# Kernel optimization log

Measured on AMD Instinct MI355X. Metric: run time of the kernel, lower is better.

## Reference

```python
import jax, jax.numpy as jnp
import numpy as np

B, L = 4, 2048
D_MODEL, D_STATE, D_CONV, EXPAND = 1024, 16, 4, 2
D_INNER = EXPAND * D_MODEL
DT_RANK = D_MODEL // 16  # mamba-ssm default dt_rank = ceil(d_model/16)


def _mamba(x, in_w, conv_w, conv_b, xproj_w, dt_w, dt_b, A_log, D, out_w):
    # x: [B, L, d_model]; faithful port of mamba_ssm.Mamba forward (slow path math)
    di, ds = A_log.shape
    dt_rank = dt_w.shape[1]
    dc = conv_w.shape[1]
    xz = x @ in_w.T                          # [B, L, 2*di]
    xi, z = jnp.split(xz, 2, axis=-1)
    # causal depthwise conv over time
    xc = jnp.swapaxes(xi, 1, 2)              # [B, di, L]
    xc = jax.lax.conv_general_dilated(
        xc, conv_w[:, None, :], (1,), [(dc - 1, 0)],
        feature_group_count=di, dimension_numbers=('NCH', 'OIH', 'NCH'))
    xc = xc + conv_b[None, :, None]
    xi = jax.nn.silu(jnp.swapaxes(xc, 1, 2))  # [B, L, di]
    proj = xi @ xproj_w.T                    # [B, L, dt_rank + 2*ds]
    dt, Bm, Cm = jnp.split(proj, [dt_rank, dt_rank + ds], axis=-1)
    delta = jax.nn.softplus(dt @ dt_w.T + dt_b)  # [B, L, di]
    A = -jnp.exp(A_log)                      # [di, ds]

    def step(h, t):
        d_t, B_t, C_t, x_t = t               # [B,di],[B,ds],[B,ds],[B,di]
        h = jnp.exp(d_t[:, :, None] * A) * h + (d_t * x_t)[:, :, None] * B_t[:, None, :]
        return h, jnp.einsum('bds,bs->bd', h, C_t)

    xs = (jnp.swapaxes(delta, 0, 1), jnp.swapaxes(Bm, 0, 1),
          jnp.swapaxes(Cm, 0, 1), jnp.swapaxes(xi, 0, 1))
    h0 = jnp.zeros((x.shape[0], di, ds), x.dtype)
    _, ys = jax.lax.scan(step, h0, xs)       # ys: [L, B, di]
    y = jnp.swapaxes(ys, 0, 1) + xi * D
    y = y * jax.nn.silu(z)
    return y @ out_w.T


def setup_inputs() -> dict:
    ks = jax.random.split(jax.random.key(0), 24)

    def p(i, shape, scale=0.02):
        return jax.random.normal(ks[i], shape, jnp.float32) * scale

    inp = {
        'x': jax.random.normal(ks[0], (B, L, D_MODEL), jnp.float32),
        'ln_g': jnp.ones((D_MODEL,), jnp.float32),
        'ln_b': jnp.zeros((D_MODEL,), jnp.float32),
        'merge_w': p(1, (D_MODEL, 2 * D_MODEL)),
        'merge_b': jnp.zeros((D_MODEL,), jnp.float32),
    }
    for j, pre in enumerate(('fwd', 'bwd')):
        o = 2 + j * 8
        inp[pre + '_in_w'] = p(o, (2 * D_INNER, D_MODEL))
        inp[pre + '_conv_w'] = p(o + 1, (D_INNER, D_CONV), 0.3)
        inp[pre + '_conv_b'] = jnp.zeros((D_INNER,), jnp.float32)
        inp[pre + '_xproj_w'] = p(o + 2, (DT_RANK + 2 * D_STATE, D_INNER))
        inp[pre + '_dt_w'] = p(o + 3, (D_INNER, DT_RANK), 0.1)
        inp[pre + '_dt_b'] = -4.0 + p(o + 4, (D_INNER,), 0.5)
        inp[pre + '_A_log'] = jnp.broadcast_to(
            jnp.log(jnp.arange(1, D_STATE + 1, dtype=jnp.float32)), (D_INNER, D_STATE)) + 0.0
        inp[pre + '_D'] = jnp.ones((D_INNER,), jnp.float32)
        inp[pre + '_out_w'] = p(o + 5, (D_MODEL, D_INNER))
    return inp


def reference(x, ln_g, ln_b, merge_w, merge_b,
              fwd_in_w, fwd_conv_w, fwd_conv_b, fwd_xproj_w, fwd_dt_w, fwd_dt_b,
              fwd_A_log, fwd_D, fwd_out_w,
              bwd_in_w, bwd_conv_w, bwd_conv_b, bwd_xproj_w, bwd_dt_w, bwd_dt_b,
              bwd_A_log, bwd_D, bwd_out_w):
    mu = jnp.mean(x, axis=-1, keepdims=True)
    var = jnp.mean(jnp.square(x - mu), axis=-1, keepdims=True)
    xn = (x - mu) / jnp.sqrt(var + 1e-5) * ln_g + ln_b
    y_f = _mamba(xn, fwd_in_w, fwd_conv_w, fwd_conv_b, fwd_xproj_w, fwd_dt_w,
                 fwd_dt_b, fwd_A_log, fwd_D, fwd_out_w)
    y_b = jnp.flip(_mamba(jnp.flip(xn, 1), bwd_in_w, bwd_conv_w, bwd_conv_b,
                          bwd_xproj_w, bwd_dt_w, bwd_dt_b, bwd_A_log, bwd_D,
                          bwd_out_w), 1)
    y = jnp.concatenate([y_f, y_b], axis=-1) @ merge_w.T + merge_b
    return x + y
```

## Files before the change

### kernel.cpp

```cpp
#include <hip/hip_runtime.h>

typedef unsigned short u16;
typedef unsigned int u32;
typedef __attribute__((ext_vector_type(8))) short short8;
typedef __attribute__((ext_vector_type(8))) u16 ushort8v;
typedef __attribute__((ext_vector_type(4))) float float4v;
typedef __attribute__((ext_vector_type(4))) u16 ushort4v;

#define SEQ_L 2048
#define NTOK 8192
#define DMODEL 1024
#define DINNER 2048
#define NCH 32
#define CHL 64

__device__ __forceinline__ float bf2f(u16 v) { return __uint_as_float(((u32)v) << 16); }
__device__ __forceinline__ u16 f2bf(float f) {
    u32 u = __float_as_uint(f);
    return (u16)((u + 0x7FFFu + ((u >> 16) & 1u)) >> 16);
}
__device__ __forceinline__ float loadf(const void* p, size_t i, bool bf) {
    return bf ? bf2f(((const u16*)p)[i]) : ((const float*)p)[i];
}
__device__ __forceinline__ void gl2lds(const void* g, void* l) {
    __builtin_amdgcn_global_load_lds(
        (const __attribute__((address_space(1))) void*)g,
        (__attribute__((address_space(3))) void*)l, 16, 0, 0);
}

#define GWAITV(N) asm volatile("s_waitcnt vmcnt(" #N ")" ::: "memory");
#define GBAR { __builtin_amdgcn_s_barrier(); asm volatile("" ::: "memory"); }

__global__ void detect_kernel(const u32* __restrict__ lng, int* __restrict__ flag) {
    if (threadIdx.x == 0) flag[0] = (lng[0] == 0x3F800000u) ? 0 : 1;
}

__global__ void cvt_kernel(const void* __restrict__ in, u16* __restrict__ out,
                           int n4, const int* __restrict__ flag) {
    int i = blockIdx.x * 256 + threadIdx.x;
    if (i >= n4) return;
    bool bf = flag[0] != 0;
    ushort4v o;
    if (bf) {
        o = ((const ushort4v*)in)[i];
    } else {
        float4v v = ((const float4v*)in)[i];
        o.x = f2bf(v.x); o.y = f2bf(v.y); o.z = f2bf(v.z); o.w = f2bf(v.w);
    }
    ((ushort4v*)out)[i] = o;
}

__global__ __launch_bounds__(256) void transpose_ow(const void* __restrict__ ow,
        u16* __restrict__ ot, const int* __restrict__ flag) {
    bool bf = flag[0] != 0;
    __shared__ u16 tile[32][33];
    int k0 = blockIdx.x * 32;
    int j0 = blockIdx.y * 32;
    int tx = threadIdx.x & 31;
    int ty = threadIdx.x >> 5;
    #pragma unroll
    for (int r = 0; r < 4; ++r) {
        int j = ty + r * 8;
        tile[j][tx] = f2bf(loadf(ow, (size_t)(j0 + j) * 2048 + k0 + tx, bf));
    }
    __syncthreads();
    #pragma unroll
    for (int r = 0; r < 4; ++r) {
        int k = ty + r * 8;
        ot[(size_t)(k0 + k) * 1024 + j0 + tx] = tile[tx][k];
    }
}

__global__ __launch_bounds__(256) void ln_kernel(const void* __restrict__ xin,
        const void* __restrict__ g, const void* __restrict__ be,
        u16* __restrict__ xn, const int* __restrict__ flag) {
    bool bf = flag[0] != 0;
    int tok = blockIdx.x;
    int tid = threadIdx.x;
    float v[4];
    if (bf) {
        ushort4v u = ((const ushort4v*)xin)[(size_t)tok * 256 + tid];
        v[0] = bf2f(u.x); v[1] = bf2f(u.y); v[2] = bf2f(u.z); v[3] = bf2f(u.w);
    } else {
        float4v f = ((const float4v*)xin)[(size_t)tok * 256 + tid];
        v[0] = f.x; v[1] = f.y; v[2] = f.z; v[3] = f.w;
    }
    float s = v[0] + v[1] + v[2] + v[3];
    float s2 = v[0]*v[0] + v[1]*v[1] + v[2]*v[2] + v[3]*v[3];
    for (int o = 1; o < 64; o <<= 1) { s += __shfl_xor(s, o); s2 += __shfl_xor(s2, o); }
    __shared__ float red[8];
    int w = tid >> 6;
    if ((tid & 63) == 0) { red[w] = s; red[4 + w] = s2; }
    __syncthreads();
    s = red[0] + red[1] + red[2] + red[3];
    s2 = red[4] + red[5] + red[6] + red[7];
    float mu = s * (1.f / 1024.f);
    float var = s2 * (1.f / 1024.f) - mu * mu;
    float rstd = rsqrtf(var + 1e-5f);
    int base = tid * 4;
    ushort4v o;
    o.x = f2bf((v[0] - mu) * rstd * loadf(g, base + 0, bf) + loadf(be, base + 0, bf));
    o.y = f2bf((v[1] - mu) * rstd * loadf(g, base + 1, bf) + loadf(be, base + 1, bf));
    o.z = f2bf((v[2] - mu) * rstd * loadf(g, base + 2, bf) + loadf(be, base + 2, bf));
    o.w = f2bf((v[3] - mu) * rstd * loadf(g, base + 3, bf) + loadf(be, base + 3, bf));
    ((ushort4v*)xn)[(size_t)tok * 256 + tid] = o;
}

__global__ __launch_bounds__(256) void build_wf(
    const void* __restrict__ dtw, const void* __restrict__ xpw,
    u16* __restrict__ wf, const int* __restrict__ flag)
{
    bool bf = flag[0] != 0;
    int n = blockIdx.x;
    int k0 = threadIdx.x * 8;
    ushort8v o;
    if (n >= DINNER) {
        int r = (n - DINNER) + 64;
        if (bf) {
            o = *(const ushort8v*)((const u16*)xpw + (size_t)r * 2048 + k0);
        } else {
            const float* p = (const float*)xpw + (size_t)r * 2048 + k0;
            #pragma unroll
            for (int j = 0; j < 8; ++j) o[j] = f2bf(p[j]);
        }
    } else {
        float acc[8];
        #pragma unroll
        for (int j = 0; j < 8; ++j) acc[j] = 0.f;
        for (int r = 0; r < 64; ++r) {
            float dw = loadf(dtw, (size_t)n * 64 + r, bf);
            if (bf) {
                ushort8v v = *(const ushort8v*)((const u16*)xpw + (size_t)r * 2048 + k0);
                #pragma unroll
                for (int j = 0; j < 8; ++j) acc[j] = fmaf(dw, bf2f(v[j]), acc[j]);
            } else {
                const float* p = (const float*)xpw + (size_t)r * 2048 + k0;
                #pragma unroll
                for (int j = 0; j < 8; ++j) acc[j] = fmaf(dw, p[j], acc[j]);
            }
        }
        #pragma unroll
        for (int j = 0; j < 8; ++j) o[j] = f2bf(acc[j]);
    }
    *(ushort8v*)(wf + (size_t)n * 2048 + k0) = o;
}

template<int EPI, bool FLIPA>
__global__ __launch_bounds__(512, 2) void gemm2x(
    const u16* __restrict__ A, int lda,
    const u16* __restrict__ W, int ldw,
    void* __restrict__ Cv, int ldc,
    int M, int N, int K,
    const void* __restrict__ bias, const void* __restrict__ resid,
    const int* __restrict__ flag)
{
    __shared__ u16 S[2][2][16384];
    bool bf = flag[0] != 0;
    int tid = threadIdx.x;
    int lane = tid & 63;
    int wave = tid >> 6;
    int wm = wave >> 2;
    int wn = wave & 3;
    int m0 = blockIdx.x * 256;
    int n0 = blockIdx.y * 256;
    int l15 = lane & 15;
    int quad = lane >> 4;

    int rloc = tid >> 3;
    int kk = ((tid & 7) ^ (rloc & 7)) << 3;
    const u16* Ag[4];
    const u16* Wg[4];
    #pragma unroll
    for (int rb = 0; rb < 4; ++rb) {
        int ar = m0 + rb * 64 + rloc;
        if (FLIPA) { int b0 = ar >> 11, t0 = ar & (SEQ_L - 1); ar = (b0 << 11) | (SEQ_L - 1 - t0); }
        Ag[rb] = A + (size_t)ar * lda + kk;
        int wr = n0 + rb * 64 + rloc; if (wr > N - 1) wr = N - 1;
        Wg[rb] = W + (size_t)wr * ldw + kk;
    }

    int s3 = l15 & 7;
    int colk[2];
    #pragma unroll
    for (int ks = 0; ks < 2; ++ks)
        colk[ks] = ((((ks ^ (s3 >> 2)) << 2) | (quad ^ (s3 & 3))) << 3);
    int abase = wm * 8192 + l15 * 64;
    int bbase = wn * 4096 + l15 * 64;

    float4v acc[8][4] = {};
    int nt = K >> 6;

#define STA(B, RB, KO) gl2lds(Ag[RB] + (KO), &S[B][0][((RB) * 512 + tid) * 8]);
#define STB(B, RB, KO) gl2lds(Wg[RB] + (KO), &S[B][1][((RB) * 512 + tid) * 8]);

    STA(0, 0, 0) STA(0, 2, 0)
    STB(0, 0, 0) STB(0, 1, 0)
    STB(0, 2, 0) STB(0, 3, 0)
    STA(0, 1, 0) STA(0, 3, 0)

    for (int t = 0; t < nt; ++t) {
        int cb = t & 1, nb = cb ^ 1;
        int ko = (t + 1) << 6;
        bool stg = (t + 1) < nt;
        const u16* sa = &S[cb][0][0];
        const u16* sb = &S[cb][1][0];

        GWAITV(2)
        GBAR
        if (stg) { STA(nb, 0, ko) STA(nb, 2, ko) }
        short8 a0[4][2];
        #pragma unroll
        for (int i = 0; i < 4; ++i)
            #pragma unroll
            for (int ks = 0; ks < 2; ++ks)
                a0[i][ks] = *(const short8*)(sa + abase + i * 1024 + colk[ks]);
        if (stg) { STB(nb, 0, ko) STB(nb, 1, ko) }
        short8 bbf[4][2];
        #pragma unroll
        for (int j = 0; j < 4; ++j)
            #pragma unroll
            for (int ks = 0; ks < 2; ++ks)
                bbf[j][ks] = *(const short8*)(sb + bbase + j * 1024 + colk[ks]);
        __builtin_amdgcn_s_setprio(1);
        #pragma unroll
        for (int i = 0; i < 4; ++i)
            #pragma unroll
            for (int j = 0; j < 4; ++j)
                #pragma unroll
                for (int ks = 0; ks < 2; ++ks)
                    acc[i][j] = __builtin_amdgcn_mfma_f32_16x16x32_bf16(a0[i][ks], bbf[j][ks], acc[i][j], 0, 0, 0);
        __builtin_amdgcn_s_setprio(0);
        if (stg) {
            STB(nb, 2, ko) STB(nb, 3, ko)
            GWAITV(6)
        } else {
            GWAITV(0)
        }
        GBAR
        #pragma unroll
        for (int i = 0; i < 4; ++i)
            #pragma unroll
            for (int ks = 0; ks < 2; ++ks)
                a0[i][ks] = *(const short8*)(sa + abase + (i + 4) * 1024 + colk[ks]);
        if (stg) { STA(nb, 1, ko) STA(nb, 3, ko) }
        __builtin_amdgcn_s_setprio(1);
        #pragma unroll
        for (int i = 0; i < 4; ++i)
            #pragma unroll
            for (int j = 0; j < 4; ++j)
                #pragma unroll
                for (int ks = 0; ks < 2; ++ks)
                    acc[i + 4][j] = __builtin_amdgcn_mfma_f32_16x16x32_bf16(a0[i][ks], bbf[j][ks], acc[i + 4][j], 0, 0, 0);
        __builtin_amdgcn_s_setprio(0);
    }
#undef STA
#undef STB

    #pragma unroll
    for (int i = 0; i < 8; ++i) {
        #pragma unroll
        for (int j = 0; j < 4; ++j) {
            #pragma unroll
            for (int r = 0; r < 4; ++r) {
                int row = m0 + wm * 128 + i * 16 + quad * 4 + r;
                int col = n0 + wn * 64 + j * 16 + l15;
                if (col < N) {
                    float v = acc[i][j][r];
                    if (EPI == 0) {
                        ((u16*)Cv)[(size_t)row * ldc + col] = f2bf(v);
                    } else if (EPI == 3) {
                        if (col < DINNER) {
                            v += loadf(bias, col, bf);
                            v = fmaxf(v, 0.f) + __logf(1.f + __expf(-fabsf(v)));
                            ((u16*)Cv)[(size_t)row * 4096 + col] = f2bf(v);
                        } else {
                            ((u16*)resid)[(size_t)row * 32 + (col - DINNER)] = f2bf(v);
                        }
                    }
                }
            }
        }
    }
}

template<int EPI, bool FLIPA>
__global__ __launch_bounds__(256) void gemm_bt(
    const u16* __restrict__ A, int lda,
    const u16* __restrict__ W, int ldw,
    void* __restrict__ Cv, int ldc,
    int M, int N, int K,
    const void* __restrict__ bias, const void* __restrict__ resid,
    const int* __restrict__ flag)
{
    __shared__ u16 As0[128 * 32];
    __shared__ u16 Ws0[128 * 32];
    __shared__ u16 As1[128 * 32];
    __shared__ u16 Ws1[128 * 32];
    bool bf = flag[0] != 0;
    int tid = threadIdx.x;
    int lane = tid & 63;
    int wave = tid >> 6;
    int wm = wave >> 1, wn = wave & 1;
    int m0 = blockIdx.x * 128;
    int n0 = blockIdx.y * 128;
    int l15 = lane & 15;
    int quad = lane >> 4;

    int c0 = tid, c1 = tid + 256;
    int row0 = c0 >> 2, row1 = c1 >> 2;
    int kk0 = ((c0 & 3) ^ ((row0 ^ (row0 >> 1)) & 3)) << 3;
    int kk1 = ((c1 & 3) ^ ((row1 ^ (row1 >> 1)) & 3)) << 3;
    int ar0 = m0 + row0, ar1 = m0 + row1;
    if (FLIPA) {
        int b0 = ar0 >> 11, t0 = ar0 & (SEQ_L - 1); ar0 = (b0 << 11) | (SEQ_L - 1 - t0);
        int b1 = ar1 >> 11, t1 = ar1 & (SEQ_L - 1); ar1 = (b1 << 11) | (SEQ_L - 1 - t1);
    }
    int wr0 = n0 + row0; if (wr0 > N - 1) wr0 = N - 1;
    int wr1 = n0 + row1; if (wr1 > N - 1) wr1 = N - 1;
    const u16* Ag0 = A + (size_t)ar0 * lda + kk0;
    const u16* Ag1 = A + (size_t)ar1 * lda + kk1;
    const u16* Wg0 = W + (size_t)wr0 * ldw + kk0;
    const u16* Wg1 = W + (size_t)wr1 * ldw + kk1;
    int sc0 = c0 * 8, sc1 = c1 * 8;

    int aoff[4], boff[4];
    #pragma unroll
    for (int i = 0; i < 4; ++i) {
        int ra = wm * 64 + i * 16 + l15;
        aoff[i] = ra * 32 + ((quad ^ ((ra ^ (ra >> 1)) & 3)) << 3);
        int rb = wn * 64 + i * 16 + l15;
        boff[i] = rb * 32 + ((quad ^ ((rb ^ (rb >> 1)) & 3)) << 3);
    }

    float4v acc[4][4] = {};
    int nt = K >> 5;

#define STAGE_T(BA, BW, KO) \
    gl2lds(Ag0 + (KO), &BA[sc0]); \
    gl2lds(Ag1 + (KO), &BA[sc1]); \
    gl2lds(Wg0 + (KO), &BW[sc0]); \
    gl2lds(Wg1 + (KO), &BW[sc1]);

#define COMPUTE_T(BA, BW) { \
    short8 af[4], bfr[4]; \
    _Pragma("unroll") \
    for (int i = 0; i < 4; ++i) af[i] = *(const short8*)&BA[aoff[i]]; \
    _Pragma("unroll") \
    for (int j = 0; j < 4; ++j) bfr[j] = *(const short8*)&BW[boff[j]]; \
    _Pragma("unroll") \
    for (int i = 0; i < 4; ++i) { \
        _Pragma("unroll") \
        for (int j = 0; j < 4; ++j) \
            acc[i][j] = __builtin_amdgcn_mfma_f32_16x16x32_bf16(af[i], bfr[j], acc[i][j], 0, 0, 0); \
    } }

#define SYNC_PIPE \
    asm volatile("s_waitcnt vmcnt(0)" ::: "memory"); \
    __builtin_amdgcn_s_barrier();

    STAGE_T(As0, Ws0, 0)
    SYNC_PIPE
    for (int t = 0; t < nt; t += 2) {
        STAGE_T(As1, Ws1, (t + 1) << 5)
        COMPUTE_T(As0, Ws0)
        SYNC_PIPE
        if (t + 2 < nt) { STAGE_T(As0, Ws0, (t + 2) << 5) }
        COMPUTE_T(As1, Ws1)
        SYNC_PIPE
    }
#undef STAGE_T
#undef COMPUTE_T
#undef SYNC_PIPE

    #pragma unroll
    for (int i = 0; i < 4; ++i) {
        #pragma unroll
        for (int j = 0; j < 4; ++j) {
            #pragma unroll
            for (int r = 0; r < 4; ++r) {
                int row = m0 + wm * 64 + i * 16 + quad * 4 + r;
                int col = n0 + wn * 64 + j * 16 + l15;
                if (col < N) {
                    float v = acc[i][j][r];
                    if (EPI == 0) {
                        ((u16*)Cv)[(size_t)row * ldc + col] = f2bf(v);
                    } else if (EPI == 2) {
                        v += loadf(bias, col, bf) + loadf(resid, (size_t)row * DMODEL + col, bf);
                        if (bf) ((u16*)Cv)[(size_t)row * ldc + col] = f2bf(v);
                        else    ((float*)Cv)[(size_t)row * ldc + col] = v;
                    } else {
                        if (bf) {
                            u16* p = (u16*)Cv + (size_t)row * ldc + col;
                            *p = f2bf(bf2f(*p) + v);
                        } else {
                            float* p = (float*)Cv + (size_t)row * ldc + col;
                            *p = *p + v;
                        }
                    }
                }
            }
        }
    }
}

__global__ __launch_bounds__(256) void conv_kernel(const u16* __restrict__ xz,
        const void* __restrict__ cw, const void* __restrict__ cb,
        u16* __restrict__ xc, const int* __restrict__ flag)
{
    bool bf = flag[0] != 0;
    int gid = blockIdx.x * 256 + threadIdx.x;
    int d = (gid & 255) << 3;
    int tok = gid >> 8;
    int t = tok & (SEQ_L - 1);
    int b = tok >> 11;
    float cwf[32], acc[8];
    if (bf) {
        const u16* p = (const u16*)cw + d * 4;
        #pragma unroll
        for (int r = 0; r < 4; ++r) {
            ushort8v v = *(const ushort8v*)(p + r * 8);
            #pragma unroll
            for (int j = 0; j < 8; ++j) cwf[r * 8 + j] = bf2f(v[j]);
        }
        ushort8v bv = *(const ushort8v*)((const u16*)cb + d);
        #pragma unroll
        for (int j = 0; j < 8; ++j) acc[j] = bf2f(bv[j]);
    } else {
        const float4v* p = (const float4v*)((const float*)cw + d * 4);
        #pragma unroll
        for (int r = 0; r < 8; ++r) {
            float4v v = p[r];
            cwf[r * 4 + 0] = v.x; cwf[r * 4 + 1] = v.y;
            cwf[r * 4 + 2] = v.z; cwf[r * 4 + 3] = v.w;
        }
        const float4v* pb = (const float4v*)((const float*)cb + d);
        float4v b0 = pb[0], b1 = pb[1];
        acc[0] = b0.x; acc[1] = b0.y; acc[2] = b0.z; acc[3] = b0.w;
        acc[4] = b1.x; acc[5] = b1.y; acc[6] = b1.z; acc[7] = b1.w;
    }
    const u16* xp = xz + (((size_t)(b * SEQ_L + t)) << 12) + d;
    #pragma unroll
    for (int k = 0; k < 4; ++k) {
        int tt = t - 3 + k;
        if (tt >= 0) {
            ushort8v xv = *(const ushort8v*)(xp + (long)(k - 3) * 4096);
            #pragma unroll
            for (int j = 0; j < 8; ++j) acc[j] = fmaf(cwf[j * 4 + k], bf2f(xv[j]), acc[j]);
        }
    }
    ushort8v o;
    #pragma unroll
    for (int j = 0; j < 8; ++j) {
        float r = acc[j] / (1.f + __expf(-acc[j]));
        o[j] = f2bf(r);
    }
    *(ushort8v*)(xc + (size_t)tok * DINNER + d) = o;
}

__global__ __launch_bounds__(256) void scan_pass1(
    const u16* __restrict__ xz, const u16* __restrict__ xc,
    const u16* __restrict__ proj, const void* __restrict__ A_log,
    float2* __restrict__ chk, const int* __restrict__ flag)
{
    bool bf = flag[0] != 0;
    int g = blockIdx.x * 256 + threadIdx.x;
    int d = g & (DINNER - 1);
    int c = (g >> 11) & (NCH - 1);
    int b = g >> 16;
    float Ac[16];
    #pragma unroll
    for (int s = 0; s < 16; ++s) Ac[s] = -__expf(loadf(A_log, (size_t)d * 16 + s, bf));
    size_t tok0 = (size_t)b * SEQ_L + c * CHL;
    const u16* dp = xz + tok0 * 4096 + d;
    const u16* xp = xc + tok0 * DINNER + d;
    const u16* bp = proj + tok0 * 32;
    float h[16];
    #pragma unroll
    for (int s = 0; s < 16; ++s) h[s] = 0.f;
    float sd = 0.f;
    for (int t = 0; t < CHL; ++t) {
        float dl = bf2f(*dp);
        float xi = bf2f(*xp);
        ushort8v bv0 = *(const ushort8v*)bp;
        ushort8v bv1 = *(const ushort8v*)(bp + 8);
        float u = dl * xi;
        #pragma unroll
        for (int s = 0; s < 16; ++s) {
            float a = __expf(dl * Ac[s]);
            float Bs = bf2f(s < 8 ? bv0[s] : bv1[s - 8]);
            h[s] = fmaf(a, h[s], u * Bs);
        }
        sd += dl;
        dp += 4096; xp += DINNER; bp += 32;
    }
    size_t base = (size_t)c * 131072 + ((size_t)b << 15) + d;
    #pragma unroll
    for (int s = 0; s < 16; ++s)
        chk[base + (size_t)s * 2048] = make_float2(__expf(Ac[s] * sd), h[s]);
}

__global__ __launch_bounds__(256) void scan_mid(float2* __restrict__ chk) {
    int g = blockIdx.x * 256 + threadIdx.x;
    float hi = 0.f;
    #pragma unroll 4
    for (int c = 0; c < NCH; ++c) {
        float2 v = chk[(size_t)c * 131072 + g];
        chk[(size_t)c * 131072 + g].x = hi;
        hi = fmaf(v.x, hi, v.y);
    }
}

__global__ __launch_bounds__(256) void scan_pass2(
    u16* __restrict__ xz, const u16* __restrict__ xc,
    const u16* __restrict__ proj, const void* __restrict__ A_log,
    const void* __restrict__ Dp, const float2* __restrict__ chk,
    const int* __restrict__ flag)
{
    bool bf = flag[0] != 0;
    int g = blockIdx.x * 256 + threadIdx.x;
    int d = g & (DINNER - 1);
    int c = (g >> 11) & (NCH - 1);
    int b = g >> 16;
    float Ac[16];
    #pragma unroll
    for (int s = 0; s < 16; ++s) Ac[s] = -__expf(loadf(A_log, (size_t)d * 16 + s, bf));
    float Dd = loadf(Dp, d, bf);
    size_t tok0 = (size_t)b * SEQ_L + c * CHL;
    const u16* dp = xz + tok0 * 4096 + d;
    const u16* xp = xc + tok0 * DINNER + d;
    const u16* bp = proj + tok0 * 32;
    u16* zp = xz + tok0 * 4096 + DINNER + d;
    size_t base = (size_t)c * 131072 + ((size_t)b << 15) + d;
    float h[16];
    #pragma unroll
    for (int s = 0; s < 16; ++s) h[s] = chk[base + (size_t)s * 2048].x;
    for (int t = 0; t < CHL; ++t) {
        float dl = bf2f(*dp);
        float xi = bf2f(*xp);
        ushort8v bv0 = *(const ushort8v*)bp;
        ushort8v bv1 = *(const ushort8v*)(bp + 8);
        ushort8v cv0 = *(const ushort8v*)(bp + 16);
        ushort8v cv1 = *(const ushort8v*)(bp + 24);
        float u = dl * xi;
        float y0 = 0.f, y1 = 0.f;
        #pragma unroll
        for (int s = 0; s < 16; ++s) {
            float a = __expf(dl * Ac[s]);
            float Bs = bf2f(s < 8 ? bv0[s] : bv1[s - 8]);
            float Cs = bf2f(s < 8 ? cv0[s] : cv1[s - 8]);
            h[s] = fmaf(a, h[s], u * Bs);
            if (s & 1) y1 = fmaf(h[s], Cs, y1); else y0 = fmaf(h[s], Cs, y0);
        }
        float y = y0 + y1 + xi * Dd;
        float z = bf2f(*zp);
        *zp = f2bf(y * (z / (1.f + __expf(-z))));
        dp += 4096; xp += DINNER; bp += 32; zp += 4096;
    }
}

extern "C" void kernel_launch(void* const* d_in, const int* in_sizes, int n_in,
                              void* d_out, int out_size, void* d_ws, size_t ws_size,
                              hipStream_t stream) {
    (void)in_sizes; (void)n_in; (void)out_size;
    const void* x = d_in[0];
    const void* ln_g = d_in[1];
    const void* ln_be = d_in[2];
    const void* merge_w = d_in[3];
    const void* merge_b = d_in[4];
    const void* in_w[2]   = {d_in[5],  d_in[14]};
    const void* conv_w[2] = {d_in[6],  d_in[15]};
    const void* conv_b[2] = {d_in[7],  d_in[16]};
    const void* xproj_w[2]= {d_in[8],  d_in[17]};
    const void* dt_w[2]   = {d_in[9],  d_in[18]};
    const void* dt_bias[2]= {d_in[10], d_in[19]};
    const void* A_log[2]  = {d_in[11], d_in[20]};
    const void* Dp[2]     = {d_in[12], d_in[21]};
    const void* out_w[2]  = {d_in[13], d_in[22]};

    char* wsb = (char*)d_ws;
    size_t off = 0;
    auto alloc = [&](size_t bytes) -> void* {
        void* p = wsb + off; off += (bytes + 255) & ~(size_t)255; return p;
    };
    int* flag     = (int*)alloc(256);
    u16* xzb      = (u16*)alloc((size_t)NTOK * 4096 * 2);
    u16* xcb      = (u16*)alloc((size_t)NTOK * 2048 * 2);
    u16* projb    = (u16*)alloc((size_t)NTOK * 32 * 2);
    float2* chk   = (float2*)alloc((size_t)NCH * 131072 * 8);
    u16* wf       = (u16*)alloc((size_t)2080 * 2048 * 2);
    u16* wof[2]   = {(u16*)alloc((size_t)1024 * 2048 * 2),
                     (u16*)alloc((size_t)1024 * 2048 * 2)};
    u16* xn       = (u16*)alloc((size_t)NTOK * DMODEL * 2);
    u16* w_mgc    = (u16*)alloc((size_t)1024 * 2048 * 2);
    u16* outT     = (u16*)alloc((size_t)2048 * 1024 * 2);
    if (off > ws_size) return;

    u16* w_in = (u16*)chk;

    detect_kernel<<<1, 64, 0, stream>>>((const u32*)ln_g, flag);
    ln_kernel<<<dim3(NTOK), 256, 0, stream>>>(x, ln_g, ln_be, xn, flag);

    auto cvt = [&](const void* src, u16* dst, int n) {
        cvt_kernel<<<dim3(n / 1024), 256, 0, stream>>>(src, dst, n / 4, flag);
    };

    cvt(merge_w, w_mgc, 1024 * 2048);
    for (int dd = 0; dd < 2; ++dd) {
        transpose_ow<<<dim3(64, 32), 256, 0, stream>>>(out_w[dd], outT, flag);
        gemm_bt<0,false><<<dim3(8, 16), 256, 0, stream>>>(
            w_mgc + dd * 1024, 2048, outT, 1024, wof[dd], 2048, 1024, 2048, 1024,
            nullptr, nullptr, flag);
    }

    for (int dd = 0; dd < 2; ++dd) {
        cvt(in_w[dd], w_in, 4096 * 1024);
        if (dd == 0)
            gemm2x<0,false><<<dim3(32,16), 512, 0, stream>>>(xn, 1024, w_in, 1024, xzb, 4096, NTOK, 4096, 1024, nullptr, nullptr, flag);
        else
            gemm2x<0,true><<<dim3(32,16), 512, 0, stream>>>(xn, 1024, w_in, 1024, xzb, 4096, NTOK, 4096, 1024, nullptr, nullptr, flag);
        conv_kernel<<<dim3((NTOK * DINNER / 8) / 256), 256, 0, stream>>>(xzb, conv_w[dd], conv_b[dd], xcb, flag);
        build_wf<<<dim3(2080), 256, 0, stream>>>(dt_w[dd], xproj_w[dd], wf, flag);
        gemm2x<3,false><<<dim3(32,9), 512, 0, stream>>>(xcb, 2048, wf, 2048, xzb, 4096, NTOK, 2080, 2048, dt_bias[dd], projb, flag);
        scan_pass1<<<dim3(1024), 256, 0, stream>>>(xzb, xcb, projb, A_log[dd], chk, flag);
        scan_mid<<<dim3(512), 256, 0, stream>>>(chk);
        scan_pass2<<<dim3(1024), 256, 0, stream>>>(xzb, xcb, projb, A_log[dd], Dp[dd], chk, flag);
        if (dd == 0)
            gemm_bt<2,false><<<dim3(64,8), 256, 0, stream>>>(xzb + DINNER, 4096, wof[0], 2048, d_out, 1024, NTOK, 1024, 2048, merge_b, x, flag);
        else
            gemm_bt<5,true><<<dim3(64,8), 256, 0, stream>>>(xzb + DINNER, 4096, wof[1], 2048, d_out, 1024, NTOK, 1024, 2048, nullptr, nullptr, flag);
    }
}
```

Baseline: 1.277 ms.

## Restructure GEMM main loop into four-phase ping-pong schedule with XCD-aware block remap

The GEMM inner loop is split into four quarter-tile phases, each loading a smaller A/B fragment set from LDS, issuing async global-to-LDS stages, then running MFMAs between barriers with explicit sched_barrier and lgkmcnt waits. This aims to overlap LDS reads, global loads and MFMA work more tightly and to cut register pressure (B fragments halved). Workgroup IDs are also remapped so consecutive blocks spread across the 8 XCDs, changing L2 locality. Extra barriers per iteration add synchronisation cost and may stall if phases are unbalanced.

```diff
diff --git a/kernel.cpp b/kernel.cpp
--- a/kernel.cpp
+++ b/kernel.cpp
@@ -30,6 +30,8 @@
 
 #define GWAITV(N) asm volatile("s_waitcnt vmcnt(" #N ")" ::: "memory");
 #define GBAR { __builtin_amdgcn_s_barrier(); asm volatile("" ::: "memory"); }
+#define LGKM0 { asm volatile("s_waitcnt lgkmcnt(0)" ::: "memory"); __builtin_amdgcn_sched_barrier(0); }
+#define SCHED0 __builtin_amdgcn_sched_barrier(0);
 
 __global__ void detect_kernel(const u32* __restrict__ lng, int* __restrict__ flag) {
     if (threadIdx.x == 0) flag[0] = (lng[0] == 0x3F800000u) ? 0 : 1;
@@ -161,8 +163,13 @@
     int wave = tid >> 6;
     int wm = wave >> 2;
     int wn = wave & 3;
-    int m0 = blockIdx.x * 256;
-    int n0 = blockIdx.y * 256;
+    int nwg = gridDim.x * gridDim.y;
+    int lin = blockIdx.y * gridDim.x + blockIdx.x;
+    int qc = nwg >> 3;
+    int id2 = (lin & 7) * qc + (lin >> 3);
+    int bx = id2 % gridDim.x, by = id2 / gridDim.x;
+    int m0 = bx * 256;
+    int n0 = by * 256;
     int l15 = lane & 15;
     int quad = lane >> 4;
 
@@ -197,6 +204,10 @@
     STB(0, 0, 0) STB(0, 1, 0)
     STB(0, 2, 0) STB(0, 3, 0)
     STA(0, 1, 0) STA(0, 3, 0)
+    GWAITV(2)
+    GBAR
+
+    short8 a[4][2], b[2][2];
 
     for (int t = 0; t < nt; ++t) {
         int cb = t & 1, nb = cb ^ 1;
@@ -205,53 +216,98 @@
         const u16* sa = &S[cb][0][0];
         const u16* sb = &S[cb][1][0];
 
-        GWAITV(2)
-        GBAR
+        #pragma unroll
+        for (int i = 0; i < 4; ++i)
+            #pragma unroll
+            for (int ks = 0; ks < 2; ++ks)
+                a[i][ks] = *(const short8*)(sa + abase + i * 1024 + colk[ks]);
+        #pragma unroll
+        for (int j = 0; j < 2; ++j)
+            #pragma unroll
+            for (int ks = 0; ks < 2; ++ks)
+                b[j][ks] = *(const short8*)(sb + bbase + j * 1024 + colk[ks]);
         if (stg) { STA(nb, 0, ko) STA(nb, 2, ko) }
-        short8 a0[4][2];
+        SCHED0
+        GBAR
+        LGKM0
+        __builtin_amdgcn_s_setprio(1);
         #pragma unroll
         for (int i = 0; i < 4; ++i)
             #pragma unroll
-            for (int ks = 0; ks < 2; ++ks)
-                a0[i][ks] = *(const short8*)(sa + abase + i * 1024 + colk[ks]);
-        if (stg) { STB(nb, 0, ko) STB(nb, 1, ko) }
-        short8 bbf[4][2];
-        #pragma unroll
-        for (int j = 0; j < 4; ++j)
-            #pragma unroll
-            for (int ks = 0; ks < 2; ++ks)
-                bbf[j][ks] = *(const short8*)(sb + bbase + j * 1024 + colk[ks]);
-        __builtin_amdgcn_s_setprio(1);
-        #pragma unroll
-        for (int i = 0; i < 4; ++i)
-            #pragma unroll
-            for (int j = 0; j < 4; ++j)
+            for (int j = 0; j < 2; ++j)
                 #pragma unroll
                 for (int ks = 0; ks < 2; ++ks)
-                    acc[i][j] = __builtin_amdgcn_mfma_f32_16x16x32_bf16(a0[i][ks], bbf[j][ks], acc[i][j], 0, 0, 0);
+                    acc[i][j] = __builtin_amdgcn_mfma_f32_16x16x32_bf16(a[i][ks], b[j][ks], acc[i][j], 0, 0, 0);
         __builtin_amdgcn_s_setprio(0);
+        GBAR
+
+        #pragma unroll
+        for (int j = 0; j < 2; ++j)
+            #pragma unroll
+            for (int ks = 0; ks < 2; ++ks)
+                b[j][ks] = *(const short8*)(sb + bbase + (j + 2) * 1024 + colk[ks]);
         if (stg) {
-            STB(nb, 2, ko) STB(nb, 3, ko)
-            GWAITV(6)
+            STB(nb, 0, ko) STB(nb, 1, ko)
+            GWAITV(4)
         } else {
             GWAITV(0)
         }
-        GBAR
+        SCHED0
+        GBAR
+        LGKM0
+        __builtin_amdgcn_s_setprio(1);
         #pragma unroll
         for (int i = 0; i < 4; ++i)
             #pragma unroll
-            for (int ks = 0; ks < 2; ++ks)
-                a0[i][ks] = *(const short8*)(sa + abase + (i + 4) * 1024 + colk[ks]);
-        if (stg) { STA(nb, 1, ko) STA(nb, 3, ko) }
-        __builtin_amdgcn_s_setprio(1);
-        #pragma unroll
-        for (int i = 0; i < 4; ++i)
-            #pragma unroll
-            for (int j = 0; j < 4; ++j)
+            for (int j = 0; j < 2; ++j)
                 #pragma unroll
                 for (int ks = 0; ks < 2; ++ks)
-                    acc[i + 4][j] = __builtin_amdgcn_mfma_f32_16x16x32_bf16(a0[i][ks], bbf[j][ks], acc[i + 4][j], 0, 0, 0);
+                    acc[i][j + 2] = __builtin_amdgcn_mfma_f32_16x16x32_bf16(a[i][ks], b[j][ks], acc[i][j + 2], 0, 0, 0);
         __builtin_amdgcn_s_setprio(0);
+        GBAR
+
+        #pragma unroll
+        for (int i = 0; i < 4; ++i)
+            #pragma unroll
+            for (int ks = 0; ks < 2; ++ks)
+                a[i][ks] = *(const short8*)(sa + abase + (i + 4) * 1024 + colk[ks]);
+        if (stg) { STB(nb, 2, ko) STB(nb, 3, ko) }
+        SCHED0
+        GBAR
+        LGKM0
+        __builtin_amdgcn_s_setprio(1);
+        #pragma unroll
+        for (int i = 0; i < 4; ++i)
+            #pragma unroll
+            for (int j = 0; j < 2; ++j)
+                #pragma unroll
+                for (int ks = 0; ks < 2; ++ks)
+                    acc[i + 4][j + 2] = __builtin_amdgcn_mfma_f32_16x16x32_bf16(a[i][ks], b[j][ks], acc[i + 4][j + 2], 0, 0, 0);
+        __builtin_amdgcn_s_setprio(0);
+        GBAR
+
+        #pragma unroll
+        for (int j = 0; j < 2; ++j)
+            #pragma unroll
+            for (int ks = 0; ks < 2; ++ks)
+                b[j][ks] = *(const short8*)(sb + bbase + j * 1024 + colk[ks]);
+        if (stg) {
+            STA(nb, 1, ko) STA(nb, 3, ko)
+            GWAITV(2)
+        }
+        SCHED0
+        GBAR
+        LGKM0
+        __builtin_amdgcn_s_setprio(1);
+        #pragma unroll
+        for (int i = 0; i < 4; ++i)
+            #pragma unroll
+            for (int j = 0; j < 2; ++j)
+                #pragma unroll
+                for (int ks = 0; ks < 2; ++ks)
+                    acc[i + 4][j] = __builtin_amdgcn_mfma_f32_16x16x32_bf16(a[i][ks], b[j][ks], acc[i + 4][j], 0, 0, 0);
+        __builtin_amdgcn_s_setprio(0);
+        GBAR
     }
 #undef STA
 #undef STB
```

After: 1.370 ms. 1.07x slower.
